# Performance work log

Measured on AMD Instinct MI355X. Metric: run time of the kernel, lower is better.

## Reference

```python
import jax, jax.numpy as jnp
import numpy as np

D_MODEL = 1024
NUM_HEADS = 16
D_KEY = D_MODEL // NUM_HEADS


def setup_inputs() -> dict:
    key = jax.random.key(0)
    ks = jax.random.split(key, 9)
    B, S = 2, 2048
    s = 1.0 / np.sqrt(D_MODEL)
    return {
        "x": jax.random.normal(ks[0], (B, S, D_MODEL), dtype=jnp.float32),
        "W_q": jax.random.normal(ks[1], (D_MODEL, D_MODEL), dtype=jnp.float32) * s,
        "b_q": jnp.zeros((D_MODEL,), dtype=jnp.float32),
        "W_k": jax.random.normal(ks[2], (D_MODEL, D_MODEL), dtype=jnp.float32) * s,
        "b_k": jnp.zeros((D_MODEL,), dtype=jnp.float32),
        "W_v": jax.random.normal(ks[3], (D_MODEL, D_MODEL), dtype=jnp.float32) * s,
        "b_v": jnp.zeros((D_MODEL,), dtype=jnp.float32),
        "W_o": jax.random.normal(ks[4], (D_MODEL, D_MODEL), dtype=jnp.float32) * s,
        "b_o": jnp.zeros((D_MODEL,), dtype=jnp.float32),
    }


def reference(x, W_q, b_q, W_k, b_k, W_v, b_v, W_o, b_o):
    B, S, _ = x.shape
    # Linear projections (torch nn.Linear: x @ W.T + b; here W stored as [in, out])
    Q = x @ W_q + b_q
    K = x @ W_k + b_k
    V = x @ W_v + b_v
    # [B, S, H, dk] -> [B, H, S, dk]
    def split_heads(t):
        return t.reshape(B, S, NUM_HEADS, D_KEY).transpose(0, 2, 1, 3)
    Q, K, V = split_heads(Q), split_heads(K), split_heads(V)
    scale = 1.0 / np.sqrt(D_KEY).astype(np.float32)
    logits = jnp.einsum("bhqd,bhkd->bhqk", Q, K) * scale  # [B,H,S,S]
    weights = jax.nn.softmax(logits, axis=-1)
    ctx = jnp.einsum("bhqk,bhkd->bhqd", weights, V)       # [B,H,S,dk]
    concat = ctx.transpose(0, 2, 1, 3).reshape(B, S, D_MODEL)
    return concat @ W_o + b_o
```

## Files before the change

### kernel.cpp

```cpp
#include <hip/hip_runtime.h>
#include <cstdint>
#include <cstddef>

#define SEQ   2048
#define NH    16
#define DK    64
#define DM    1024
#define MTOT  4096
#define QSCALE (0.125f * 1.44269504088896f)

typedef __attribute__((ext_vector_type(8))) short           short8;
typedef __attribute__((ext_vector_type(8))) unsigned short  ushort8;
typedef __attribute__((ext_vector_type(4))) unsigned short  ushort4v;
typedef __attribute__((ext_vector_type(2))) unsigned int    uint2v;
typedef __attribute__((ext_vector_type(4))) unsigned int    uint4v;
typedef __attribute__((ext_vector_type(4))) float           float4v;
typedef unsigned short u16;
typedef unsigned int   u32;

__device__ inline float4v mfma16(short8 a, short8 b, float4v c) {
    return __builtin_amdgcn_mfma_f32_16x16x32_bf16(a, b, c, 0, 0, 0);
}
__device__ inline u16 f2bf(float f) {
    u32 u = __float_as_uint(f);
    u += 0x7fffu + ((u >> 16) & 1u);
    return (u16)(u >> 16);
}
__device__ inline u32 pkbf(float a, float b) {
    u32 r;
    asm("v_cvt_pk_bf16_f32 %0, %1, %2" : "=v"(r) : "v"(a), "v"(b));
    return r;
}
__device__ inline float ex2(float x) {
    float r;
    asm("v_exp_f32 %0, %1" : "=v"(r) : "v"(x));
    return r;
}
__device__ inline void pl32swap(u32& a, u32& b) {
    asm("v_permlane32_swap_b32 %0, %1" : "+v"(a), "+v"(b));
}
__device__ inline void pl16swap(u32& a, u32& b) {
    asm("v_permlane16_swap_b32 %0, %1" : "+v"(a), "+v"(b));
}
__device__ inline void gld16(const void* g, void* lds) {
    __builtin_amdgcn_global_load_lds(
        (const __attribute__((address_space(1))) u32*)g,
        (__attribute__((address_space(3))) u32*)lds, 16, 0, 0);
}

__global__ __launch_bounds__(256)
void convert_x(const float* __restrict__ x, u16* __restrict__ xb)
{
    const int i = blockIdx.x * 256 + threadIdx.x;
    const float4v a = ((const float4v*)x)[2 * i];
    const float4v b = ((const float4v*)x)[2 * i + 1];
    ushort8 o;
    #pragma unroll
    for (int j = 0; j < 4; j++) { o[j] = f2bf(a[j]); o[4 + j] = f2bf(b[j]); }
    ((ushort8*)xb)[i] = o;
}

__global__ __launch_bounds__(256)
void transpose_w(const float* __restrict__ W0, const float* __restrict__ W1,
                 const float* __restrict__ W2, const float* __restrict__ W3,
                 u16* __restrict__ T0, u16* __restrict__ T1,
                 u16* __restrict__ T2, u16* __restrict__ T3)
{
    __shared__ u16 t[64][68];
    const float* W; u16* T;
    switch (blockIdx.z) {
        case 0: W = W0; T = T0; break;
        case 1: W = W1; T = T1; break;
        case 2: W = W2; T = T2; break;
        default: W = W3; T = T3; break;
    }
    const int n0 = blockIdx.x * 64, k0 = blockIdx.y * 64;
    const int r  = threadIdx.x >> 4;
    const int c4 = (threadIdx.x & 15) * 4;
    #pragma unroll
    for (int i = 0; i < 4; i++) {
        float4v v = *(const float4v*)&W[(size_t)(k0 + r + i * 16) * DM + n0 + c4];
        #pragma unroll
        for (int j = 0; j < 4; j++) t[r + i * 16][c4 + j] = f2bf(v[j]);
    }
    __syncthreads();
    #pragma unroll
    for (int i = 0; i < 4; i++) {
        const int rr = r + i * 16;
        ushort4v o;
        #pragma unroll
        for (int j = 0; j < 4; j++) o[j] = t[c4 + j][rr];
        *(ushort4v*)&T[(size_t)(n0 + rr) * DM + k0 + c4] = o;
    }
}

template<int TM, int MODE>
__global__ __launch_bounds__(TM * 4)
void gemm_bt(const u16* __restrict__ A, const u16* __restrict__ WT,
             const float* __restrict__ bq, const float* __restrict__ bk,
             const float* __restrict__ bv,
             void* __restrict__ out0, u16* __restrict__ outK, u16* __restrict__ outV)
{
    constexpr int NT = TM * 4;
    __shared__ u16 Al[TM][64];
    __shared__ u16 Bl[128][64];
    const int tid  = threadIdx.x;
    const int lane = tid & 63, w = tid >> 6;
    const int quad = lane >> 4, l16 = lane & 15;
    const int n0 = blockIdx.x * 128, m0 = blockIdx.y * TM;
    const int wm = (TM == 128) ? (w >> 2) * 64 : 0;
    const int wn = (TM == 128) ? (w & 3) * 32 : w * 32;

    float4v acc[4][2] = {};

    for (int k0 = 0; k0 < DM; k0 += 64) {
        __syncthreads();
        #pragma unroll
        for (int j = 0; j < TM * 8 / NT; j++) {
            const int c = j * NT + tid;
            const int row = c >> 3, kc = c & 7;
            gld16(A + (size_t)(m0 + row) * DM + k0 + ((kc ^ (row & 7)) * 8),
                  &Al[0][0] + (size_t)(j * NT + w * 64) * 8);
        }
        #pragma unroll
        for (int j = 0; j < 1024 / NT; j++) {
            const int c = j * NT + tid;
            const int row = c >> 3, kc = c & 7;
            gld16(WT + (size_t)(n0 + row) * DM + k0 + ((kc ^ (row & 7)) * 8),
                  &Bl[0][0] + (size_t)(j * NT + w * 64) * 8);
        }
        __syncthreads();
        #pragma unroll
        for (int u = 0; u < 2; u++) {
            short8 af[4], bf[2];
            #pragma unroll
            for (int mi = 0; mi < 4; mi++) {
                const int row = wm + mi * 16 + l16;
                af[mi] = *(const short8*)&Al[row][((4 * u + quad) ^ (row & 7)) * 8];
            }
            #pragma unroll
            for (int ni = 0; ni < 2; ni++) {
                const int row = wn + ni * 16 + l16;
                bf[ni] = *(const short8*)&Bl[row][((4 * u + quad) ^ (row & 7)) * 8];
            }
            #pragma unroll
            for (int mi = 0; mi < 4; mi++)
                #pragma unroll
                for (int ni = 0; ni < 2; ni++)
                    acc[mi][ni] = mfma16(af[mi], bf[ni], acc[mi][ni]);
        }
    }

    if constexpr (MODE == 0) {
        float* out = (float*)out0;
        #pragma unroll
        for (int ni = 0; ni < 2; ni++) {
            const int col = n0 + wn + ni * 16 + l16;
            const float bb = bq[col];
            #pragma unroll
            for (int mi = 0; mi < 4; mi++)
                #pragma unroll
                for (int r = 0; r < 4; r++) {
                    const int row = m0 + wm + mi * 16 + quad * 4 + r;
                    out[(size_t)row * DM + col] = acc[mi][ni][r] + bb;
                }
        }
    } else {
        const int seg = n0 >> 10;
        u16* outp = (seg == 0) ? (u16*)out0 : (seg == 1 ? outK : outV);
        const float* bias = (seg == 0) ? bq : (seg == 1 ? bk : bv);
        const float scl = (seg == 0) ? QSCALE : 1.0f;
        if (seg < 2) {
            #pragma unroll
            for (int ni = 0; ni < 2; ni++) {
                const int col = (n0 & 1023) + wn + ni * 16 + l16;
                const float bb = bias[col];
                const int h = col >> 6, d = col & 63;
                #pragma unroll
                for (int mi = 0; mi < 4; mi++)
                    #pragma unroll
                    for (int r = 0; r < 4; r++) {
                        const int row = m0 + wm + mi * 16 + quad * 4 + r;
                        const int b = row >> 11, s = row & (SEQ - 1);
                        outp[(((size_t)(b * NH + h) * SEQ + s) << 6) + d] =
                            f2bf((acc[mi][ni][r] + bb) * scl);
                    }
            }
        } else {
            #pragma unroll
            for (int ni = 0; ni < 2; ni++) {
                const int col = (n0 & 1023) + wn + ni * 16 + l16;
                const float bb = bias[col];
                const int h = col >> 6, d = col & 63;
                #pragma unroll
                for (int mi = 0; mi < 4; mi++) {
                    const int row0 = m0 + wm + mi * 16 + quad * 4;
                    const int b = row0 >> 11, s = row0 & (SEQ - 1);
                    uint2v pv;
                    pv[0] = pkbf(acc[mi][ni][0] + bb, acc[mi][ni][1] + bb);
                    pv[1] = pkbf(acc[mi][ni][2] + bb, acc[mi][ni][3] + bb);
                    *(uint2v*)&outp[(((size_t)((b * NH + h) * DK + d)) << 11) + s] = pv;
                }
            }
        }
    }
}

__global__ __launch_bounds__(512, 4)
void attn_kernel(const u16* __restrict__ Q, const u16* __restrict__ K,
                 const u16* __restrict__ VT, u16* __restrict__ Ctx)
{
    __shared__ u16 Kl[2][2][32][64];
    __shared__ u16 Vl[2][2][64][32];
    __shared__ float Xl[4][64][17];

    const int tid  = threadIdx.x;
    const int lane = tid & 63, w = tid >> 6;
    const int wq = w & 3, wgrp = w >> 2;
    const int quad = lane >> 4, l16 = lane & 15;
    const int qt = blockIdx.x;
    const int bh = blockIdx.y;
    const size_t head = (size_t)bh * SEQ * DK;

    short8 qf[2][2];
    #pragma unroll
    for (int g = 0; g < 2; g++) {
        const size_t qrow = head + (size_t)(qt * 128 + wq * 32 + g * 16 + l16) * DK;
        qf[g][0] = *(const short8*)(Q + qrow + quad * 8);
        qf[g][1] = *(const short8*)(Q + qrow + 32 + quad * 8);
    }

    float4v acc[2][4] = {};
    float l_part[2] = {0.f, 0.f};

    const int sh = tid >> 8;
    const int rK = (tid >> 3) & 31, cK = tid & 7;
    const int dV = (tid >> 2) & 63, cV = tid & 3;
    const int sVk = (dV & 3) ^ ((dV >> 2) & 3);
    const u16* const Kg = K  + head + (size_t)(sh * 1024 + rK) * DK + (cK ^ (rK & 7)) * 8;
    const u16* const Vg = VT + head + (size_t)dV * SEQ + sh * 1024 + (cV ^ sVk) * 8;
    u16* const Kdst = &Kl[0][0][0][0] + tid * 8;
    u16* const Vdst = &Vl[0][0][0][0] + tid * 8;

    gld16(Kg, Kdst);
    gld16(Vg, Vdst);

    for (int it = 0; it < 32; it++) {
        const int cur = it & 1;
        __syncthreads();
        if (it + 1 < 32) {
            gld16(Kg + (size_t)(it + 1) * 32 * DK, Kdst + (cur ^ 1) * 4096);
            gld16(Vg + (size_t)(it + 1) * 32,      Vdst + (cur ^ 1) * 4096);
        }

        short8 kf[2][2];
        #pragma unroll
        for (int t = 0; t < 2; t++) {
            const int row = t * 16 + l16;
            kf[t][0] = *(const short8*)&Kl[cur][wgrp][row][(quad ^ (row & 7)) * 8];
            kf[t][1] = *(const short8*)&Kl[cur][wgrp][row][((4 + quad) ^ (row & 7)) * 8];
        }
        float4v z[2][2];
        __builtin_amdgcn_s_setprio(1);
        #pragma unroll
        for (int t = 0; t < 2; t++)
            #pragma unroll
            for (int g = 0; g < 2; g++) {
                float4v zz = {};
                zz = mfma16(kf[t][0], qf[g][0], zz);
                zz = mfma16(kf[t][1], qf[g][1], zz);
                z[t][g] = zz;
            }
        __builtin_amdgcn_s_setprio(0);

        short8 pf[2];
        #pragma unroll
        for (int g = 0; g < 2; g++) {
            float p[2][4];
            #pragma unroll
            for (int t = 0; t < 2; t++) {
                p[t][0] = ex2(z[t][g][0]); p[t][1] = ex2(z[t][g][1]);
                p[t][2] = ex2(z[t][g][2]); p[t][3] = ex2(z[t][g][3]);
                l_part[g] += (p[t][0] + p[t][1]) + (p[t][2] + p[t][3]);
            }
            u32 A = pkbf(p[0][0], p[0][1]);
            u32 B = pkbf(p[0][2], p[0][3]);
            u32 C = pkbf(p[1][0], p[1][1]);
            u32 D = pkbf(p[1][2], p[1][3]);
            pl32swap(A, C); pl16swap(A, C);
            pl32swap(B, D); pl16swap(B, D);
            uint4v pw; pw[0] = A; pw[1] = B; pw[2] = C; pw[3] = D;
            pf[g] = __builtin_bit_cast(short8, pw);
        }

        __builtin_amdgcn_s_setprio(1);
        #pragma unroll
        for (int t = 0; t < 4; t++) {
            const int d = t * 16 + l16;
            const short8 vf =
                *(const short8*)&Vl[cur][wgrp][d][(quad ^ ((d & 3) ^ ((d >> 2) & 3))) * 8];
            acc[0][t] = mfma16(vf, pf[0], acc[0][t]);
            acc[1][t] = mfma16(vf, pf[1], acc[1][t]);
        }
        __builtin_amdgcn_s_setprio(0);
    }

    #pragma unroll
    for (int g = 0; g < 2; g++) {
        l_part[g] += __shfl_xor(l_part[g], 16);
        l_part[g] += __shfl_xor(l_part[g], 32);
    }

    float ltot[2];
    #pragma unroll
    for (int p = 0; p < 2; p++) {
        __syncthreads();
        if (wgrp == 1) {
            #pragma unroll
            for (int g = 0; g < 2; g++)
                #pragma unroll
                for (int tt = 0; tt < 2; tt++)
                    #pragma unroll
                    for (int r = 0; r < 4; r++)
                        Xl[wq][lane][g * 8 + tt * 4 + r] = acc[g][2 * p + tt][r];
            Xl[wq][lane][16] = l_part[p];
        }
        __syncthreads();
        if (wgrp == 0) {
            #pragma unroll
            for (int g = 0; g < 2; g++)
                #pragma unroll
                for (int tt = 0; tt < 2; tt++)
                    #pragma unroll
                    for (int r = 0; r < 4; r++)
                        acc[g][2 * p + tt][r] += Xl[wq][lane][g * 8 + tt * 4 + r];
            ltot[p] = l_part[p] + Xl[wq][lane][16];
        }
    }

    if (wgrp == 0) {
        const int b = bh >> 4, h = bh & 15;
        #pragma unroll
        for (int g = 0; g < 2; g++) {
            const float rl = 1.0f / ltot[g];
            const int s = qt * 128 + wq * 32 + g * 16 + l16;
            u16* dst = Ctx + (size_t)(b * SEQ + s) * DM + h * 64 + quad * 4;
            #pragma unroll
            for (int t = 0; t < 4; t++) {
                uint2v ov;
                ov[0] = pkbf(acc[g][t][0] * rl, acc[g][t][1] * rl);
                ov[1] = pkbf(acc[g][t][2] * rl, acc[g][t][3] * rl);
                *(uint2v*)&dst[t * 16] = ov;
            }
        }
    }
}

extern "C" void kernel_launch(void* const* d_in, const int* in_sizes, int n_in,
                              void* d_out, int out_size, void* d_ws, size_t ws_size,
                              hipStream_t stream)
{
    const float* x   = (const float*)d_in[0];
    const float* W_q = (const float*)d_in[1];
    const float* b_q = (const float*)d_in[2];
    const float* W_k = (const float*)d_in[3];
    const float* b_k = (const float*)d_in[4];
    const float* W_v = (const float*)d_in[5];
    const float* b_v = (const float*)d_in[6];
    const float* W_o = (const float*)d_in[7];
    const float* b_o = (const float*)d_in[8];

    u16* xb  = (u16*)d_ws;
    u16* WT  = xb + (size_t)MTOT * DM;
    u16* WTo = WT + (size_t)3 * DM * DM;
    u16* VTb = WTo + (size_t)DM * DM;
    u16* Cb  = xb;
    u16* Qb  = (u16*)d_out;
    u16* Kb  = Qb + (size_t)MTOT * DM;

    convert_x<<<2048, 256, 0, stream>>>(x, xb);
    transpose_w<<<dim3(16, 16, 4), 256, 0, stream>>>(
        W_q, W_k, W_v, W_o, WT, WT + (size_t)DM * DM, WT + (size_t)2 * DM * DM, WTo);
    gemm_bt<128, 1><<<dim3(24, 32), 512, 0, stream>>>(xb, WT, b_q, b_k, b_v, Qb, Kb, VTb);
    attn_kernel<<<dim3(SEQ / 128, 2 * NH), 512, 0, stream>>>(Qb, Kb, VTb, Cb);
    gemm_bt<64, 0><<<dim3(8, 64), 256, 0, stream>>>(Cb, WTo, b_o, nullptr, nullptr,
                                                    (float*)d_out, nullptr, nullptr);
}
```

Before: 186.5 us.

## Remap workgroups XCD-aware and use 512 threads for output projection GEMM

Block indices in both GEMM and attention kernels are remapped so that consecutive logical tiles land on the same XCD (grouping by wgid mod 8), aiming to improve L2 reuse of shared K/V and weight tiles on the multi-die MI355X. The output projection GEMM now runs with 512 threads per block, each wave computing a smaller M-fragment (MF=TM/32), which raises the wave count per tile. The remap relies on grid sizes being divisible by 8, and the smaller per-wave work may reduce MFMA-to-load ratio.

```diff
diff --git a/kernel.cpp b/kernel.cpp
--- a/kernel.cpp
+++ b/kernel.cpp
@@ -95,23 +95,30 @@
 }
 
 template<int TM, int MODE>
-__global__ __launch_bounds__(TM * 4)
+__global__ __launch_bounds__(512)
 void gemm_bt(const u16* __restrict__ A, const u16* __restrict__ WT,
              const float* __restrict__ bq, const float* __restrict__ bk,
              const float* __restrict__ bv,
              void* __restrict__ out0, u16* __restrict__ outK, u16* __restrict__ outV)
 {
-    constexpr int NT = TM * 4;
+    constexpr int NT = 512;
+    constexpr int MF = TM / 32;
     __shared__ u16 Al[TM][64];
     __shared__ u16 Bl[128][64];
     const int tid  = threadIdx.x;
     const int lane = tid & 63, w = tid >> 6;
     const int quad = lane >> 4, l16 = lane & 15;
-    const int n0 = blockIdx.x * 128, m0 = blockIdx.y * TM;
-    const int wm = (TM == 128) ? (w >> 2) * 64 : 0;
-    const int wn = (TM == 128) ? (w & 3) * 32 : w * 32;
-
-    float4v acc[4][2] = {};
+
+    const int nxb  = gridDim.x;
+    const int wgid = blockIdx.y * nxb + blockIdx.x;
+    const int per  = (nxb * gridDim.y) >> 3;
+    const int nl   = (wgid & 7) * per + (wgid >> 3);
+    const int n0 = (nl % nxb) * 128, m0 = (nl / nxb) * TM;
+
+    const int wm = (w >> 2) * (TM / 2);
+    const int wn = (w & 3) * 32;
+
+    float4v acc[MF][2] = {};
 
     for (int k0 = 0; k0 < DM; k0 += 64) {
         __syncthreads();
@@ -132,9 +139,9 @@
         __syncthreads();
         #pragma unroll
         for (int u = 0; u < 2; u++) {
-            short8 af[4], bf[2];
-            #pragma unroll
-            for (int mi = 0; mi < 4; mi++) {
+            short8 af[MF], bf[2];
+            #pragma unroll
+            for (int mi = 0; mi < MF; mi++) {
                 const int row = wm + mi * 16 + l16;
                 af[mi] = *(const short8*)&Al[row][((4 * u + quad) ^ (row & 7)) * 8];
             }
@@ -144,7 +151,7 @@
                 bf[ni] = *(const short8*)&Bl[row][((4 * u + quad) ^ (row & 7)) * 8];
             }
             #pragma unroll
-            for (int mi = 0; mi < 4; mi++)
+            for (int mi = 0; mi < MF; mi++)
                 #pragma unroll
                 for (int ni = 0; ni < 2; ni++)
                     acc[mi][ni] = mfma16(af[mi], bf[ni], acc[mi][ni]);
@@ -158,7 +165,7 @@
             const int col = n0 + wn + ni * 16 + l16;
             const float bb = bq[col];
             #pragma unroll
-            for (int mi = 0; mi < 4; mi++)
+            for (int mi = 0; mi < MF; mi++)
                 #pragma unroll
                 for (int r = 0; r < 4; r++) {
                     const int row = m0 + wm + mi * 16 + quad * 4 + r;
@@ -177,7 +184,7 @@
                 const float bb = bias[col];
                 const int h = col >> 6, d = col & 63;
                 #pragma unroll
-                for (int mi = 0; mi < 4; mi++)
+                for (int mi = 0; mi < MF; mi++)
                     #pragma unroll
                     for (int r = 0; r < 4; r++) {
                         const int row = m0 + wm + mi * 16 + quad * 4 + r;
@@ -193,7 +200,7 @@
                 const float bb = bias[col];
                 const int h = col >> 6, d = col & 63;
                 #pragma unroll
-                for (int mi = 0; mi < 4; mi++) {
+                for (int mi = 0; mi < MF; mi++) {
                     const int row0 = m0 + wm + mi * 16 + quad * 4;
                     const int b = row0 >> 11, s = row0 & (SEQ - 1);
                     uint2v pv;
@@ -218,8 +225,11 @@
     const int lane = tid & 63, w = tid >> 6;
     const int wq = w & 3, wgrp = w >> 2;
     const int quad = lane >> 4, l16 = lane & 15;
-    const int qt = blockIdx.x;
-    const int bh = blockIdx.y;
+
+    const int wgid = blockIdx.y * 16 + blockIdx.x;
+    const int nlin = (wgid & 7) * 64 + (wgid >> 3);
+    const int qt = nlin & 15;
+    const int bh = nlin >> 4;
     const size_t head = (size_t)bh * SEQ * DK;
 
     short8 qf[2][2];
@@ -383,6 +393,6 @@
         W_q, W_k, W_v, W_o, WT, WT + (size_t)DM * DM, WT + (size_t)2 * DM * DM, WTo);
     gemm_bt<128, 1><<<dim3(24, 32), 512, 0, stream>>>(xb, WT, b_q, b_k, b_v, Qb, Kb, VTb);
     attn_kernel<<<dim3(SEQ / 128, 2 * NH), 512, 0, stream>>>(Qb, Kb, VTb, Cb);
-    gemm_bt<64, 0><<<dim3(8, 64), 256, 0, stream>>>(Cb, WTo, b_o, nullptr, nullptr,
+    gemm_bt<64, 0><<<dim3(8, 64), 512, 0, stream>>>(Cb, WTo, b_o, nullptr, nullptr,
                                                     (float*)d_out, nullptr, nullptr);
 }
```

Measured after the change: 186.9 us. Within noise of the previous version (+0.2%).
